# Optimization experiments

Measured on AMD Instinct MI355X. Metric: run time of the kernel, lower is better.

The kernel has to match this reference:

```python
import jax, jax.numpy as jnp
import numpy as np

N_NODES = 100000
N_EDGES = 1600000
IN_DIM = 128
HID = 64
HEADS = 1
NEG_SLOPE = 0.2


def setup_inputs() -> dict:
    key = jax.random.key(0)
    ks = jax.random.split(key, 12)
    def xavier(k, shape):
        fan_in, fan_out = shape[-2], shape[-1]
        lim = jnp.sqrt(6.0 / (fan_in + fan_out))
        return jax.random.uniform(k, shape, jnp.float32, -lim, lim)
    x = jax.random.normal(ks[0], (N_NODES, IN_DIM), jnp.float32)
    edge_index = jax.random.randint(ks[1], (2, N_EDGES), 0, N_NODES, jnp.int64)
    # layer 0: in 128 -> heads*hid (64)
    W0 = xavier(ks[2], (IN_DIM, HEADS * HID))
    al0 = xavier(ks[3], (1, HEADS, HID))
    ar0 = xavier(ks[4], (1, HEADS, HID))
    # layer 1: in heads*hid (64) -> 64
    W1 = xavier(ks[5], (HEADS * HID, HEADS * HID))
    al1 = xavier(ks[6], (1, HEADS, HID))
    ar1 = xavier(ks[7], (1, HEADS, HID))
    # post_mp: Linear(64,64) -> Linear(64,64)
    Wp1 = xavier(ks[8], (HEADS * HID, HID))
    bp1 = jnp.zeros((HID,), jnp.float32)
    Wp2 = xavier(ks[9], (HID, HID))
    bp2 = jnp.zeros((HID,), jnp.float32)
    return {"x": x, "edge_index": edge_index, "W0": W0, "al0": al0, "ar0": ar0,
            "W1": W1, "al1": al1, "ar1": ar1, "Wp1": Wp1, "bp1": bp1,
            "Wp2": Wp2, "bp2": bp2}


def gat_layer(x, W, att_l, att_r, src, dst, n_nodes):
    H, C = att_l.shape[1], att_l.shape[2]
    # lin_l == lin_r (shared weight), no bias
    xh = (x @ W).reshape(n_nodes, H, C)            # [N,H,C]
    alpha_l = jnp.sum(xh * att_l, axis=-1)         # [N,H]
    alpha_r = jnp.sum(xh * att_r, axis=-1)         # [N,H]
    # per-edge logit: alpha_i (dst) + alpha_j (src)
    a = alpha_l[src] + alpha_r[dst]                # [E,H]
    a = jnp.where(a >= 0, a, NEG_SLOPE * a)        # leaky_relu
    # segment softmax over incoming edges of each dst node
    amax = jax.ops.segment_max(a, dst, num_segments=n_nodes)
    e = jnp.exp(a - amax[dst])
    denom = jax.ops.segment_sum(e, dst, num_segments=n_nodes)
    alpha = e / (denom[dst] + 1e-16)               # [E,H]
    msg = xh[src] * alpha[:, :, None]              # [E,H,C]
    out = jax.ops.segment_sum(msg, dst, num_segments=n_nodes)  # [N,H,C]
    return out.reshape(n_nodes, H * C)


def reference(x, edge_index, W0, al0, ar0, W1, al1, ar1, Wp1, bp1, Wp2, bp2):
    src, dst = edge_index[0], edge_index[1]
    n = x.shape[0]
    h = gat_layer(x, W0, al0, ar0, src, dst, n)
    h = jax.nn.relu(h)
    h = gat_layer(h, W1, al1, ar1, src, dst, n)
    h = jax.nn.relu(h)
    # post_mp (dropout inactive in eval)
    h = h @ Wp1 + bp1
    h = h @ Wp2 + bp2
    return h  # emb=True -> return embedding
```

## Files before the change

kernel.cpp:

```cpp
#include <hip/hip_runtime.h>
#include <math.h>

#define NEG_SLOPE 0.2f
#define CAP 8192

typedef _Float16 half8 __attribute__((ext_vector_type(8)));
typedef _Float16 half4v __attribute__((ext_vector_type(4)));
typedef float float4v __attribute__((ext_vector_type(4)));

__global__ void setup_misc(const float* __restrict__ W0, const float* __restrict__ W1,
                           const float* __restrict__ Wp1, const float* __restrict__ Wp2,
                           _Float16* __restrict__ W0T, _Float16* __restrict__ W1T,
                           _Float16* __restrict__ Wp1T, _Float16* __restrict__ Wp2T,
                           int* __restrict__ cursor, int NB) {
    const int tid = threadIdx.x;
    if (blockIdx.x == 4) {
        for (int t = tid; t < NB; t += 256) cursor[t] = t * CAP;
        return;
    }
    __shared__ float lds[128 * 64];
    const float* src; _Float16* dstp; int K;
    switch (blockIdx.x) {
        case 0: src = W0;  dstp = W0T;  K = 128; break;
        case 1: src = W1;  dstp = W1T;  K = 64;  break;
        case 2: src = Wp1; dstp = Wp1T; K = 64;  break;
        default: src = Wp2; dstp = Wp2T; K = 64; break;
    }
    for (int i = tid; i < K * 64; i += 256) lds[i] = src[i];
    __syncthreads();
    for (int i = tid; i < K * 64; i += 256) {
        int n = i / K, k = i % K;
        dstp[i] = (_Float16)lds[k * 64 + n];
    }
}

__device__ __forceinline__ void bin_body(const int* __restrict__ src,
                                         const int* __restrict__ dst,
                                         int* __restrict__ cursor,
                                         unsigned int* __restrict__ packed,
                                         int E, int NB, int bid) {
    __shared__ int h[512];
    const int tid = threadIdx.x;
    for (int t = tid; t < NB; t += 256) h[t] = 0;
    __syncthreads();
    const int base = bid * 4096;
    const int lim = min(base + 4096, E);
    int dreg[16];
    int cnt = 0;
    for (int i = base + tid; i < lim; i += 256) dreg[cnt++] = dst[i];
    for (int k = 0; k < cnt; ++k) atomicAdd(&h[dreg[k] >> 8], 1);
    __syncthreads();
    for (int t = tid; t < NB; t += 256) {
        int c = h[t];
        h[t] = c ? atomicAdd(&cursor[t], c) : 0;
    }
    __syncthreads();
    cnt = 0;
    for (int i = base + tid; i < lim; i += 256) {
        int d = dreg[cnt++];
        int s = src[i];
        int pos = atomicAdd(&h[d >> 8], 1);
        packed[pos] = ((unsigned int)(d & 255) << 24) | (unsigned int)s;
    }
}

__device__ __forceinline__ void gemm0_body(const float* __restrict__ X,
                                           const _Float16* __restrict__ WT,
                                           const float* __restrict__ alw,
                                           const float* __restrict__ arw,
                                           _Float16* __restrict__ XH,
                                           float* __restrict__ AL, float* __restrict__ AR,
                                           int N, int bid) {
    const int wid = threadIdx.x >> 6, lane = threadIdx.x & 63;
    const int rowbase = bid * 64 + wid * 16;
    const int idx16 = lane & 15;
    const int g = lane >> 4;
    const int mrow = rowbase + idx16;
    const bool mvalid = (mrow < N);

    float4v acc[4];
    #pragma unroll
    for (int n = 0; n < 4; ++n) acc[n] = float4v{0.f, 0.f, 0.f, 0.f};

    #pragma unroll
    for (int ks = 0; ks < 4; ++ks) {
        const int k0 = ks * 32 + g * 8;
        half8 a = {};
        if (mvalid) {
            const float* xp = X + (size_t)mrow * 128 + k0;
            float4v lo = *reinterpret_cast<const float4v*>(xp);
            float4v hi = *reinterpret_cast<const float4v*>(xp + 4);
            #pragma unroll
            for (int i = 0; i < 4; ++i) {
                a[i] = (_Float16)lo[i];
                a[i + 4] = (_Float16)hi[i];
            }
        }
        #pragma unroll
        for (int n = 0; n < 4; ++n) {
            const half8 b = *reinterpret_cast<const half8*>(WT + (size_t)(n * 16 + idx16) * 128 + k0);
            acc[n] = __builtin_amdgcn_mfma_f32_16x16x32_f16(a, b, acc[n], 0, 0, 0);
        }
    }

    float alv[4], arv[4];
    #pragma unroll
    for (int n = 0; n < 4; ++n) { alv[n] = alw[n * 16 + idx16]; arv[n] = arw[n * 16 + idx16]; }
    #pragma unroll
    for (int r = 0; r < 4; ++r) {
        const int row = rowbase + g * 4 + r;
        if (row < N) {
            float pl = 0.f, pr = 0.f;
            #pragma unroll
            for (int n = 0; n < 4; ++n) {
                float vv = acc[n][r];
                XH[(size_t)row * 64 + n * 16 + idx16] = (_Float16)vv;
                pl = fmaf(vv, alv[n], pl);
                pr = fmaf(vv, arv[n], pr);
            }
            pl += __shfl_xor(pl, 1); pr += __shfl_xor(pr, 1);
            pl += __shfl_xor(pl, 2); pr += __shfl_xor(pr, 2);
            pl += __shfl_xor(pl, 4); pr += __shfl_xor(pr, 4);
            pl += __shfl_xor(pl, 8); pr += __shfl_xor(pr, 8);
            if (idx16 == 0) { AL[row] = pl; AR[row] = pr; }
        }
    }
}

__global__ void gemm0_and_bin(const float* __restrict__ X,
                              const _Float16* __restrict__ W0T,
                              const float* __restrict__ alw, const float* __restrict__ arw,
                              _Float16* __restrict__ XH0, float* __restrict__ AL0,
                              float* __restrict__ AR0,
                              const int* __restrict__ src, const int* __restrict__ dst,
                              int* __restrict__ cursor, unsigned int* __restrict__ packed,
                              int N, int E, int NB, int geb) {
    if ((int)blockIdx.x < geb)
        bin_body(src, dst, cursor, packed, E, NB, blockIdx.x);
    else
        gemm0_body(X, W0T, alw, arw, XH0, AL0, AR0, N, blockIdx.x - geb);
}

__global__ void bucket_sort(const unsigned int* __restrict__ packed,
                            const int* __restrict__ cursor,
                            int* __restrict__ csr, int2* __restrict__ rr, int N) {
    __shared__ int hist[256], cur[256];
    __shared__ int wsum[4], woff[4];
    const int tid = threadIdx.x, wid = tid >> 6, lane = tid & 63;
    const int b = blockIdx.x;
    const int beg = b * CAP;
    const int end = cursor[b];
    hist[tid] = 0;
    __syncthreads();
    for (int i = beg + tid; i < end; i += 256)
        atomicAdd(&hist[packed[i] >> 24], 1);
    __syncthreads();
    int v = hist[tid];
    int x = v;
    #pragma unroll
    for (int off = 1; off < 64; off <<= 1) {
        int t = __shfl_up(x, off);
        if (lane >= off) x += t;
    }
    if (lane == 63) wsum[wid] = x;
    __syncthreads();
    if (tid == 0) {
        int acc = 0;
        #pragma unroll
        for (int w = 0; w < 4; ++w) { woff[w] = acc; acc += wsum[w]; }
    }
    __syncthreads();
    int excl = woff[wid] + x - v;
    int node = (b << 8) + tid;
    if (node < N) rr[node] = make_int2(beg + excl, v);
    cur[tid] = excl;
    __syncthreads();
    for (int i = beg + tid; i < end; i += 256) {
        unsigned int p = packed[i];
        int pos = atomicAdd(&cur[p >> 24], 1);
        csr[beg + pos] = (int)(p & 0xFFFFFFu);
    }
}


__device__ __forceinline__ void agg_phase(const int2* __restrict__ rr,
                                          const int* __restrict__ csr,
                                          const float* __restrict__ ALp,
                                          const float* __restrict__ ARp,
                                          const _Float16* __restrict__ XHp,
                                          _Float16* ts, int nb, int N) {
    const int tid = threadIdx.x;
    const int l = tid & 15, grp = tid >> 4;
    const int node = nb + grp;
    float4v acc = {0.f, 0.f, 0.f, 0.f};
    float inv = 0.0f;
    if (node < N) {
        const int2 r = rr[node];
        const int beg = r.x, end = r.x + r.y;
        const float ar = ARp[node];
        float s = 0.f;
        for (int cbeg = beg; cbeg < end; cbeg += 16) {
            const int e = cbeg + l;
            const bool valid = (e < end);
            const int sidx = valid ? csr[e] : 0;
            float a = ALp[sidx] + ar;
            a = (a >= 0.0f) ? a : NEG_SLOPE * a;
            const float ex = valid ? __expf(a) : 0.0f;
            s += ex;
            #pragma unroll
            for (int j = 0; j < 16; ++j) {
                const float wgt = __shfl(ex, j, 16);
                const int si = __shfl(sidx, j, 16);
                const half4v h = *reinterpret_cast<const half4v*>(XHp + (size_t)si * 64 + l * 4);
                acc[0] = fmaf((float)h[0], wgt, acc[0]);
                acc[1] = fmaf((float)h[1], wgt, acc[1]);
                acc[2] = fmaf((float)h[2], wgt, acc[2]);
                acc[3] = fmaf((float)h[3], wgt, acc[3]);
            }
        }
        s += __shfl_xor(s, 1); s += __shfl_xor(s, 2);
        s += __shfl_xor(s, 4); s += __shfl_xor(s, 8);
        inv = 1.0f / (s + 1e-16f);
    }
    half4v o;
    o[0] = (_Float16)fmaxf(acc[0] * inv, 0.f);
    o[1] = (_Float16)fmaxf(acc[1] * inv, 0.f);
    o[2] = (_Float16)fmaxf(acc[2] * inv, 0.f);
    o[3] = (_Float16)fmaxf(acc[3] * inv, 0.f);
    const int hoff = (grp * 128 + ((l * 8) ^ ((grp & 7) << 4))) >> 1;
    *reinterpret_cast<half4v*>(ts + hoff) = o;
    __syncthreads();
}

__device__ __forceinline__ half8 ts_afrag(const _Float16* ts, int row, int kb) {
    return *reinterpret_cast<const half8*>(ts + ((row * 128 + (kb ^ ((row & 7) << 4))) >> 1));
}

__global__ void agg_gemm_mid(const int2* __restrict__ rr, const int* __restrict__ csr,
                             const float* __restrict__ AL0, const float* __restrict__ AR0,
                             const _Float16* __restrict__ XH0,
                             const _Float16* __restrict__ W1T,
                             const float* __restrict__ al1w, const float* __restrict__ ar1w,
                             _Float16* __restrict__ XH1, float* __restrict__ AL1,
                             float* __restrict__ AR1, int N) {
    __shared__ _Float16 ts[16 * 64];
    const int nb = blockIdx.x * 16;
    agg_phase(rr, csr, AL0, AR0, XH0, ts, nb, N);
    if (threadIdx.x >= 64) return;

    const int lane = threadIdx.x;
    const int idx16 = lane & 15, g = lane >> 4;
    float alv[4], arv[4];
    #pragma unroll
    for (int n = 0; n < 4; ++n) { alv[n] = al1w[n * 16 + idx16]; arv[n] = ar1w[n * 16 + idx16]; }

    float4v acc[4];
    #pragma unroll
    for (int n = 0; n < 4; ++n) acc[n] = float4v{0.f, 0.f, 0.f, 0.f};
    #pragma unroll
    for (int ks = 0; ks < 2; ++ks) {
        const half8 a = ts_afrag(ts, idx16, ks * 64 + g * 16);
        const int k0 = ks * 32 + g * 8;
        #pragma unroll
        for (int n = 0; n < 4; ++n) {
            const half8 b = *reinterpret_cast<const half8*>(W1T + (size_t)(n * 16 + idx16) * 64 + k0);
            acc[n] = __builtin_amdgcn_mfma_f32_16x16x32_f16(a, b, acc[n], 0, 0, 0);
        }
    }
    #pragma unroll
    for (int r = 0; r < 4; ++r) {
        const int row = nb + g * 4 + r;
        if (row < N) {
            float pl = 0.f, pr = 0.f;
            #pragma unroll
            for (int n = 0; n < 4; ++n) {
                float vv = acc[n][r];
                XH1[(size_t)row * 64 + n * 16 + idx16] = (_Float16)vv;
                pl = fmaf(vv, alv[n], pl);
                pr = fmaf(vv, arv[n], pr);
            }
            pl += __shfl_xor(pl, 1); pr += __shfl_xor(pr, 1);
            pl += __shfl_xor(pl, 2); pr += __shfl_xor(pr, 2);
            pl += __shfl_xor(pl, 4); pr += __shfl_xor(pr, 4);
            pl += __shfl_xor(pl, 8); pr += __shfl_xor(pr, 8);
            if (idx16 == 0) { AL1[row] = pl; AR1[row] = pr; }
        }
    }
}

__global__ void agg_post(const int2* __restrict__ rr, const int* __restrict__ csr,
                         const float* __restrict__ AL1, const float* __restrict__ AR1,
                         const _Float16* __restrict__ XH1,
                         const _Float16* __restrict__ Wp1T, const float* __restrict__ bp1,
                         const _Float16* __restrict__ Wp2T, const float* __restrict__ bp2,
                         float* __restrict__ OUT, int N) {
    __shared__ _Float16 ts[16 * 64];
    __shared__ _Float16 tls[16][72];
    const int nb = blockIdx.x * 16;
    agg_phase(rr, csr, AL1, AR1, XH1, ts, nb, N);
    if (threadIdx.x >= 64) return;

    const int lane = threadIdx.x;
    const int idx16 = lane & 15, g = lane >> 4;

    float4v acc1[4];
    #pragma unroll
    for (int n = 0; n < 4; ++n) acc1[n] = float4v{0.f, 0.f, 0.f, 0.f};
    #pragma unroll
    for (int ks = 0; ks < 2; ++ks) {
        const half8 a = ts_afrag(ts, idx16, ks * 64 + g * 16);
        const int k0 = ks * 32 + g * 8;
        #pragma unroll
        for (int n = 0; n < 4; ++n) {
            const half8 b = *reinterpret_cast<const half8*>(Wp1T + (size_t)(n * 16 + idx16) * 64 + k0);
            acc1[n] = __builtin_amdgcn_mfma_f32_16x16x32_f16(a, b, acc1[n], 0, 0, 0);
        }
    }
    #pragma unroll
    for (int r = 0; r < 4; ++r)
        #pragma unroll
        for (int n = 0; n < 4; ++n)
            tls[g * 4 + r][n * 16 + idx16] = (_Float16)(acc1[n][r] + bp1[n * 16 + idx16]);

    float4v acc2[4];
    #pragma unroll
    for (int n = 0; n < 4; ++n) acc2[n] = float4v{0.f, 0.f, 0.f, 0.f};
    #pragma unroll
    for (int ks = 0; ks < 2; ++ks) {
        const int k0 = ks * 32 + g * 8;
        const half8 a = *reinterpret_cast<const half8*>(&tls[idx16][k0]);
        #pragma unroll
        for (int n = 0; n < 4; ++n) {
            const half8 b = *reinterpret_cast<const half8*>(Wp2T + (size_t)(n * 16 + idx16) * 64 + k0);
            acc2[n] = __builtin_amdgcn_mfma_f32_16x16x32_f16(a, b, acc2[n], 0, 0, 0);
        }
    }
    #pragma unroll
    for (int r = 0; r < 4; ++r) {
        const int row = nb + g * 4 + r;
        if (row < N) {
            #pragma unroll
            for (int n = 0; n < 4; ++n)
                OUT[(size_t)row * 64 + n * 16 + idx16] = acc2[n][r] + bp2[n * 16 + idx16];
        }
    }
}

extern "C" void kernel_launch(void* const* d_in, const int* in_sizes, int n_in,
                              void* d_out, int out_size, void* d_ws, size_t ws_size,
                              hipStream_t stream) {
    const float* x   = (const float*)d_in[0];
    const int*   ei  = (const int*)d_in[1];
    const float* W0  = (const float*)d_in[2];
    const float* al0 = (const float*)d_in[3];
    const float* ar0 = (const float*)d_in[4];
    const float* W1  = (const float*)d_in[5];
    const float* al1 = (const float*)d_in[6];
    const float* ar1 = (const float*)d_in[7];
    const float* Wp1 = (const float*)d_in[8];
    const float* bp1 = (const float*)d_in[9];
    const float* Wp2 = (const float*)d_in[10];
    const float* bp2 = (const float*)d_in[11];
    float* out = (float*)d_out;

    const int N = in_sizes[0] / 128;
    const int E = in_sizes[1] / 2;
    const int* src = ei;
    const int* dst = ei + E;
    const int NB = (N + 255) >> 8;

    char* w = (char*)d_ws;
    _Float16* XH0  = (_Float16*)w;     w += sizeof(_Float16) * (size_t)N * 64;
    _Float16* XH1  = (_Float16*)w;     w += sizeof(_Float16) * (size_t)N * 64;
    float*  AL0    = (float*)w;        w += sizeof(float) * N;
    float*  AR0    = (float*)w;        w += sizeof(float) * N;
    float*  AL1    = (float*)w;        w += sizeof(float) * N;
    float*  AR1    = (float*)w;        w += sizeof(float) * N;
    int2*   rr     = (int2*)w;         w += sizeof(int2) * N;
    int*    csr    = (int*)w;          w += sizeof(int) * (size_t)NB * CAP;
    unsigned int* packed = (unsigned int*)w; w += sizeof(unsigned int) * (size_t)NB * CAP;
    int*    cursor = (int*)w;          w += sizeof(int) * 512;
    _Float16* W0T  = (_Float16*)w;     w += sizeof(_Float16) * 128 * 64;
    _Float16* W1T  = (_Float16*)w;     w += sizeof(_Float16) * 64 * 64;
    _Float16* Wp1T = (_Float16*)w;     w += sizeof(_Float16) * 64 * 64;
    _Float16* Wp2T = (_Float16*)w;

    dim3 blk(256);
    const int gn64 = (N + 63) / 64;
    const int gn16 = (N + 15) / 16;
    const int geb  = (E + 4095) / 4096;

    setup_misc<<<5, blk, 0, stream>>>(W0, W1, Wp1, Wp2, W0T, W1T, Wp1T, Wp2T,
                                      cursor, NB);

    gemm0_and_bin<<<geb + gn64, blk, 0, stream>>>(x, W0T, al0, ar0, XH0, AL0, AR0,
                                                  src, dst, cursor, packed,
                                                  N, E, NB, geb);

    bucket_sort<<<NB, blk, 0, stream>>>(packed, cursor, csr, rr, N);

    agg_gemm_mid<<<gn16, blk, 0, stream>>>(rr, csr, AL0, AR0, XH0,
                                           W1T, al1, ar1, XH1, AL1, AR1, N);

    agg_post<<<gn16, blk, 0, stream>>>(rr, csr, AL1, AR1, XH1,
                                       Wp1T, bp1, Wp2T, bp2, out, N);
}
```

Baseline: 150.5 us.

## Group nodes by degree class via permutation to balance aggregation work

```diff
diff --git a/kernel.cpp b/kernel.cpp
--- a/kernel.cpp
+++ b/kernel.cpp
@@ -12,10 +12,11 @@
                            const float* __restrict__ Wp1, const float* __restrict__ Wp2,
                            _Float16* __restrict__ W0T, _Float16* __restrict__ W1T,
                            _Float16* __restrict__ Wp1T, _Float16* __restrict__ Wp2T,
-                           int* __restrict__ cursor, int NB) {
+                           int* __restrict__ cursor, int* __restrict__ cls16, int NB) {
     const int tid = threadIdx.x;
     if (blockIdx.x == 4) {
         for (int t = tid; t < NB; t += 256) cursor[t] = t * CAP;
+        if (tid < 16) cls16[tid] = 0;
         return;
     }
     __shared__ float lds[128 * 64];
@@ -34,16 +35,14 @@
     }
 }
 
-__device__ __forceinline__ void bin_body(const int* __restrict__ src,
-                                         const int* __restrict__ dst,
-                                         int* __restrict__ cursor,
-                                         unsigned int* __restrict__ packed,
-                                         int E, int NB, int bid) {
+__global__ void bin_k(const int* __restrict__ src, const int* __restrict__ dst,
+                      int* __restrict__ cursor, unsigned int* __restrict__ packed,
+                      int E, int NB) {
     __shared__ int h[512];
     const int tid = threadIdx.x;
     for (int t = tid; t < NB; t += 256) h[t] = 0;
     __syncthreads();
-    const int base = bid * 4096;
+    const int base = blockIdx.x * 4096;
     const int lim = min(base + 4096, E);
     int dreg[16];
     int cnt = 0;
@@ -61,6 +60,51 @@
         int s = src[i];
         int pos = atomicAdd(&h[d >> 8], 1);
         packed[pos] = ((unsigned int)(d & 255) << 24) | (unsigned int)s;
+    }
+}
+
+__device__ __forceinline__ void sort_body(const unsigned int* __restrict__ packed,
+                                          const int* __restrict__ cursor,
+                                          int* __restrict__ csr, int2* __restrict__ rr,
+                                          int* __restrict__ classhist, int N, int b) {
+    __shared__ int hist[256], cur[256];
+    __shared__ int wsum[4], woff[4];
+    __shared__ int chist[8];
+    const int tid = threadIdx.x, wid = tid >> 6, lane = tid & 63;
+    const int beg = b * CAP;
+    const int end = cursor[b];
+    hist[tid] = 0;
+    if (tid < 8) chist[tid] = 0;
+    __syncthreads();
+    for (int i = beg + tid; i < end; i += 256)
+        atomicAdd(&hist[packed[i] >> 24], 1);
+    __syncthreads();
+    int v = hist[tid];
+    const int node = (b << 8) + tid;
+    if (node < N) atomicAdd(&chist[min((v + 15) >> 4, 7)], 1);
+    int x = v;
+    #pragma unroll
+    for (int off = 1; off < 64; off <<= 1) {
+        int t = __shfl_up(x, off);
+        if (lane >= off) x += t;
+    }
+    if (lane == 63) wsum[wid] = x;
+    __syncthreads();
+    if (tid == 0) {
+        int acc = 0;
+        #pragma unroll
+        for (int w = 0; w < 4; ++w) { woff[w] = acc; acc += wsum[w]; }
+    }
+    __syncthreads();
+    if (tid < 8 && chist[tid]) atomicAdd(&classhist[tid], chist[tid]);
+    int excl = woff[wid] + x - v;
+    if (node < N) rr[node] = make_int2(beg + excl, v);
+    cur[tid] = excl;
+    __syncthreads();
+    for (int i = beg + tid; i < end; i += 256) {
+        unsigned int p = packed[i];
+        int pos = atomicAdd(&cur[p >> 24], 1);
+        csr[beg + pos] = (int)(p & 0xFFFFFFu);
     }
 }
 
@@ -127,74 +171,64 @@
     }
 }
 
-__global__ void gemm0_and_bin(const float* __restrict__ X,
-                              const _Float16* __restrict__ W0T,
-                              const float* __restrict__ alw, const float* __restrict__ arw,
-                              _Float16* __restrict__ XH0, float* __restrict__ AL0,
-                              float* __restrict__ AR0,
-                              const int* __restrict__ src, const int* __restrict__ dst,
-                              int* __restrict__ cursor, unsigned int* __restrict__ packed,
-                              int N, int E, int NB, int geb) {
-    if ((int)blockIdx.x < geb)
-        bin_body(src, dst, cursor, packed, E, NB, blockIdx.x);
+__global__ void sort_and_gemm0(const unsigned int* __restrict__ packed,
+                               const int* __restrict__ cursor,
+                               int* __restrict__ csr, int2* __restrict__ rr,
+                               int* __restrict__ classhist,
+                               const float* __restrict__ X,
+                               const _Float16* __restrict__ W0T,
+                               const float* __restrict__ alw, const float* __restrict__ arw,
+                               _Float16* __restrict__ XH0, float* __restrict__ AL0,
+                               float* __restrict__ AR0, int N, int NB) {
+    if ((int)blockIdx.x < NB)
+        sort_body(packed, cursor, csr, rr, classhist, N, blockIdx.x);
     else
-        gemm0_body(X, W0T, alw, arw, XH0, AL0, AR0, N, blockIdx.x - geb);
-}
-
-__global__ void bucket_sort(const unsigned int* __restrict__ packed,
-                            const int* __restrict__ cursor,
-                            int* __restrict__ csr, int2* __restrict__ rr, int N) {
-    __shared__ int hist[256], cur[256];
-    __shared__ int wsum[4], woff[4];
-    const int tid = threadIdx.x, wid = tid >> 6, lane = tid & 63;
-    const int b = blockIdx.x;
-    const int beg = b * CAP;
-    const int end = cursor[b];
-    hist[tid] = 0;
-    __syncthreads();
-    for (int i = beg + tid; i < end; i += 256)
-        atomicAdd(&hist[packed[i] >> 24], 1);
-    __syncthreads();
-    int v = hist[tid];
-    int x = v;
-    #pragma unroll
-    for (int off = 1; off < 64; off <<= 1) {
-        int t = __shfl_up(x, off);
-        if (lane >= off) x += t;
-    }
-    if (lane == 63) wsum[wid] = x;
-    __syncthreads();
-    if (tid == 0) {
-        int acc = 0;
-        #pragma unroll
-        for (int w = 0; w < 4; ++w) { woff[w] = acc; acc += wsum[w]; }
-    }
-    __syncthreads();
-    int excl = woff[wid] + x - v;
-    int node = (b << 8) + tid;
-    if (node < N) rr[node] = make_int2(beg + excl, v);
-    cur[tid] = excl;
-    __syncthreads();
-    for (int i = beg + tid; i < end; i += 256) {
-        unsigned int p = packed[i];
-        int pos = atomicAdd(&cur[p >> 24], 1);
-        csr[beg + pos] = (int)(p & 0xFFFFFFu);
+        gemm0_body(X, W0T, alw, arw, XH0, AL0, AR0, N, blockIdx.x - NB);
+}
+
+__global__ void class_scatter(const int2* __restrict__ rr,
+                              const int* __restrict__ classhist,
+                              int* __restrict__ classOffset,
+                              int* __restrict__ perm, int N) {
+    __shared__ int h[8], cur[8];
+    const int tid = threadIdx.x;
+    const int node = blockIdx.x * 256 + tid;
+    if (tid < 8) h[tid] = 0;
+    __syncthreads();
+    int c = -1;
+    if (node < N) {
+        c = min((rr[node].y + 15) >> 4, 7);
+        atomicAdd(&h[c], 1);
+    }
+    __syncthreads();
+    if (tid < 8) {
+        int cnt = h[tid];
+        cur[tid] = cnt ? atomicAdd(&classOffset[tid], cnt) : 0;
+    }
+    __syncthreads();
+    if (node < N) {
+        int cb = 0;
+        for (int k = 0; k < c; ++k) cb += classhist[k];
+        int pos = cb + atomicAdd(&cur[c], 1);
+        perm[pos] = node;
     }
 }
 
 
 __device__ __forceinline__ void agg_phase(const int2* __restrict__ rr,
                                           const int* __restrict__ csr,
+                                          const int* __restrict__ perm,
                                           const float* __restrict__ ALp,
                                           const float* __restrict__ ARp,
                                           const _Float16* __restrict__ XHp,
                                           _Float16* ts, int nb, int N) {
     const int tid = threadIdx.x;
     const int l = tid & 15, grp = tid >> 4;
-    const int node = nb + grp;
+    const int nidx = nb + grp;
     float4v acc = {0.f, 0.f, 0.f, 0.f};
     float inv = 0.0f;
-    if (node < N) {
+    if (nidx < N) {
+        const int node = perm[nidx];
         const int2 r = rr[node];
         const int beg = r.x, end = r.x + r.y;
         const float ar = ARp[node];
@@ -237,6 +271,7 @@
 }
 
 __global__ void agg_gemm_mid(const int2* __restrict__ rr, const int* __restrict__ csr,
+                             const int* __restrict__ perm,
                              const float* __restrict__ AL0, const float* __restrict__ AR0,
                              const _Float16* __restrict__ XH0,
                              const _Float16* __restrict__ W1T,
@@ -245,7 +280,7 @@
                              float* __restrict__ AR1, int N) {
     __shared__ _Float16 ts[16 * 64];
     const int nb = blockIdx.x * 16;
-    agg_phase(rr, csr, AL0, AR0, XH0, ts, nb, N);
+    agg_phase(rr, csr, perm, AL0, AR0, XH0, ts, nb, N);
     if (threadIdx.x >= 64) return;
 
     const int lane = threadIdx.x;
@@ -269,13 +304,14 @@
     }
     #pragma unroll
     for (int r = 0; r < 4; ++r) {
-        const int row = nb + g * 4 + r;
-        if (row < N) {
+        const int idx = nb + g * 4 + r;
+        if (idx < N) {
+            const int prow = perm[idx];
             float pl = 0.f, pr = 0.f;
             #pragma unroll
             for (int n = 0; n < 4; ++n) {
                 float vv = acc[n][r];
-                XH1[(size_t)row * 64 + n * 16 + idx16] = (_Float16)vv;
+                XH1[(size_t)prow * 64 + n * 16 + idx16] = (_Float16)vv;
                 pl = fmaf(vv, alv[n], pl);
                 pr = fmaf(vv, arv[n], pr);
             }
@@ -283,12 +319,13 @@
             pl += __shfl_xor(pl, 2); pr += __shfl_xor(pr, 2);
             pl += __shfl_xor(pl, 4); pr += __shfl_xor(pr, 4);
             pl += __shfl_xor(pl, 8); pr += __shfl_xor(pr, 8);
-            if (idx16 == 0) { AL1[row] = pl; AR1[row] = pr; }
+            if (idx16 == 0) { AL1[prow] = pl; AR1[prow] = pr; }
         }
     }
 }
 
 __global__ void agg_post(const int2* __restrict__ rr, const int* __restrict__ csr,
+                         const int* __restrict__ perm,
                          const float* __restrict__ AL1, const float* __restrict__ AR1,
                          const _Float16* __restrict__ XH1,
                          const _Float16* __restrict__ Wp1T, const float* __restrict__ bp1,
@@ -297,7 +334,7 @@
     __shared__ _Float16 ts[16 * 64];
     __shared__ _Float16 tls[16][72];
     const int nb = blockIdx.x * 16;
-    agg_phase(rr, csr, AL1, AR1, XH1, ts, nb, N);
+    agg_phase(rr, csr, perm, AL1, AR1, XH1, ts, nb, N);
     if (threadIdx.x >= 64) return;
 
     const int lane = threadIdx.x;
@@ -337,11 +374,12 @@
     }
     #pragma unroll
     for (int r = 0; r < 4; ++r) {
-        const int row = nb + g * 4 + r;
-        if (row < N) {
+        const int idx = nb + g * 4 + r;
+        if (idx < N) {
+            const int prow = perm[idx];
             #pragma unroll
             for (int n = 0; n < 4; ++n)
-                OUT[(size_t)row * 64 + n * 16 + idx16] = acc2[n][r] + bp2[n * 16 + idx16];
+                OUT[(size_t)prow * 64 + n * 16 + idx16] = acc2[n][r] + bp2[n * 16 + idx16];
         }
     }
 }
@@ -380,28 +418,35 @@
     int*    csr    = (int*)w;          w += sizeof(int) * (size_t)NB * CAP;
     unsigned int* packed = (unsigned int*)w; w += sizeof(unsigned int) * (size_t)NB * CAP;
     int*    cursor = (int*)w;          w += sizeof(int) * 512;
+    int*    cls16  = (int*)w;          w += sizeof(int) * 16;
+    int*    perm   = (int*)w;          w += sizeof(int) * N;
     _Float16* W0T  = (_Float16*)w;     w += sizeof(_Float16) * 128 * 64;
     _Float16* W1T  = (_Float16*)w;     w += sizeof(_Float16) * 64 * 64;
     _Float16* Wp1T = (_Float16*)w;     w += sizeof(_Float16) * 64 * 64;
     _Float16* Wp2T = (_Float16*)w;
+    int* classhist   = cls16;
+    int* classOffset = cls16 + 8;
 
     dim3 blk(256);
     const int gn64 = (N + 63) / 64;
     const int gn16 = (N + 15) / 16;
+    const int gn256 = (N + 255) / 256;
     const int geb  = (E + 4095) / 4096;
 
     setup_misc<<<5, blk, 0, stream>>>(W0, W1, Wp1, Wp2, W0T, W1T, Wp1T, Wp2T,
-                                      cursor, NB);
-
-    gemm0_and_bin<<<geb + gn64, blk, 0, stream>>>(x, W0T, al0, ar0, XH0, AL0, AR0,
-                                                  src, dst, cursor, packed,
-                                                  N, E, NB, geb);
-
-    bucket_sort<<<NB, blk, 0, stream>>>(packed, cursor, csr, rr, N);
-
-    agg_gemm_mid<<<gn16, blk, 0, stream>>>(rr, csr, AL0, AR0, XH0,
+                                      cursor, cls16, NB);
+
+    bin_k<<<geb, blk, 0, stream>>>(src, dst, cursor, packed, E, NB);
+
+    sort_and_gemm0<<<NB + gn64, blk, 0, stream>>>(packed, cursor, csr, rr, classhist,
+                                                  x, W0T, al0, ar0, XH0, AL0, AR0,
+                                                  N, NB);
+
+    class_scatter<<<gn256, blk, 0, stream>>>(rr, classhist, classOffset, perm, N);
+
+    agg_gemm_mid<<<gn16, blk, 0, stream>>>(rr, csr, perm, AL0, AR0, XH0,
                                            W1T, al1, ar1, XH1, AL1, AR1, N);
 
-    agg_post<<<gn16, blk, 0, stream>>>(rr, csr, AL1, AR1, XH1,
+    agg_post<<<gn16, blk, 0, stream>>>(rr, csr, perm, AL1, AR1, XH1,
                                        Wp1T, bp1, Wp2T, bp2, out, N);
 }
```

Measured after the change: 155.8 us. 1.04x slower.

## Reorder nodes by in-degree class within buckets to balance aggregation groups

Applied to the files above, without the earlier changes.

```diff
diff --git a/kernel.cpp b/kernel.cpp
--- a/kernel.cpp
+++ b/kernel.cpp
@@ -143,19 +143,29 @@
 
 __global__ void bucket_sort(const unsigned int* __restrict__ packed,
                             const int* __restrict__ cursor,
-                            int* __restrict__ csr, int2* __restrict__ rr, int N) {
+                            int* __restrict__ csr, int2* __restrict__ rr,
+                            int* __restrict__ perm, int N) {
     __shared__ int hist[256], cur[256];
     __shared__ int wsum[4], woff[4];
+    __shared__ int chist[8], coff[8], crank[8];
     const int tid = threadIdx.x, wid = tid >> 6, lane = tid & 63;
     const int b = blockIdx.x;
     const int beg = b * CAP;
     const int end = cursor[b];
     hist[tid] = 0;
+    if (tid < 8) { chist[tid] = 0; crank[tid] = 0; }
     __syncthreads();
     for (int i = beg + tid; i < end; i += 256)
         atomicAdd(&hist[packed[i] >> 24], 1);
     __syncthreads();
-    int v = hist[tid];
+    const int v = hist[tid];
+    const int node = (b << 8) + tid;
+    const int c = min((v + 15) >> 4, 7);
+    int rank = 0;
+    if (node < N) {
+        atomicAdd(&chist[c], 1);
+        rank = atomicAdd(&crank[c], 1);
+    }
     int x = v;
     #pragma unroll
     for (int off = 1; off < 64; off <<= 1) {
@@ -168,11 +178,16 @@
         int acc = 0;
         #pragma unroll
         for (int w = 0; w < 4; ++w) { woff[w] = acc; acc += wsum[w]; }
+        acc = 0;
+        #pragma unroll
+        for (int k = 0; k < 8; ++k) { coff[k] = acc; acc += chist[k]; }
     }
     __syncthreads();
     int excl = woff[wid] + x - v;
-    int node = (b << 8) + tid;
-    if (node < N) rr[node] = make_int2(beg + excl, v);
+    if (node < N) {
+        rr[node] = make_int2(beg + excl, v);
+        perm[(b << 8) + coff[c] + rank] = node;
+    }
     cur[tid] = excl;
     __syncthreads();
     for (int i = beg + tid; i < end; i += 256) {
@@ -185,16 +200,18 @@
 
 __device__ __forceinline__ void agg_phase(const int2* __restrict__ rr,
                                           const int* __restrict__ csr,
+                                          const int* __restrict__ perm,
                                           const float* __restrict__ ALp,
                                           const float* __restrict__ ARp,
                                           const _Float16* __restrict__ XHp,
                                           _Float16* ts, int nb, int N) {
     const int tid = threadIdx.x;
     const int l = tid & 15, grp = tid >> 4;
-    const int node = nb + grp;
+    const int nidx = nb + grp;
     float4v acc = {0.f, 0.f, 0.f, 0.f};
     float inv = 0.0f;
-    if (node < N) {
+    if (nidx < N) {
+        const int node = perm[nidx];
         const int2 r = rr[node];
         const int beg = r.x, end = r.x + r.y;
         const float ar = ARp[node];
@@ -237,6 +254,7 @@
 }
 
 __global__ void agg_gemm_mid(const int2* __restrict__ rr, const int* __restrict__ csr,
+                             const int* __restrict__ perm,
                              const float* __restrict__ AL0, const float* __restrict__ AR0,
                              const _Float16* __restrict__ XH0,
                              const _Float16* __restrict__ W1T,
@@ -245,7 +263,7 @@
                              float* __restrict__ AR1, int N) {
     __shared__ _Float16 ts[16 * 64];
     const int nb = blockIdx.x * 16;
-    agg_phase(rr, csr, AL0, AR0, XH0, ts, nb, N);
+    agg_phase(rr, csr, perm, AL0, AR0, XH0, ts, nb, N);
     if (threadIdx.x >= 64) return;
 
     const int lane = threadIdx.x;
@@ -269,13 +287,14 @@
     }
     #pragma unroll
     for (int r = 0; r < 4; ++r) {
-        const int row = nb + g * 4 + r;
-        if (row < N) {
+        const int idx = nb + g * 4 + r;
+        if (idx < N) {
+            const int prow = perm[idx];
             float pl = 0.f, pr = 0.f;
             #pragma unroll
             for (int n = 0; n < 4; ++n) {
                 float vv = acc[n][r];
-                XH1[(size_t)row * 64 + n * 16 + idx16] = (_Float16)vv;
+                XH1[(size_t)prow * 64 + n * 16 + idx16] = (_Float16)vv;
                 pl = fmaf(vv, alv[n], pl);
                 pr = fmaf(vv, arv[n], pr);
             }
@@ -283,12 +302,13 @@
             pl += __shfl_xor(pl, 2); pr += __shfl_xor(pr, 2);
             pl += __shfl_xor(pl, 4); pr += __shfl_xor(pr, 4);
             pl += __shfl_xor(pl, 8); pr += __shfl_xor(pr, 8);
-            if (idx16 == 0) { AL1[row] = pl; AR1[row] = pr; }
+            if (idx16 == 0) { AL1[prow] = pl; AR1[prow] = pr; }
         }
     }
 }
 
 __global__ void agg_post(const int2* __restrict__ rr, const int* __restrict__ csr,
+                         const int* __restrict__ perm,
                          const float* __restrict__ AL1, const float* __restrict__ AR1,
                          const _Float16* __restrict__ XH1,
                          const _Float16* __restrict__ Wp1T, const float* __restrict__ bp1,
@@ -297,7 +317,7 @@
     __shared__ _Float16 ts[16 * 64];
     __shared__ _Float16 tls[16][72];
     const int nb = blockIdx.x * 16;
-    agg_phase(rr, csr, AL1, AR1, XH1, ts, nb, N);
+    agg_phase(rr, csr, perm, AL1, AR1, XH1, ts, nb, N);
     if (threadIdx.x >= 64) return;
 
     const int lane = threadIdx.x;
@@ -337,11 +357,12 @@
     }
     #pragma unroll
     for (int r = 0; r < 4; ++r) {
-        const int row = nb + g * 4 + r;
-        if (row < N) {
+        const int idx = nb + g * 4 + r;
+        if (idx < N) {
+            const int prow = perm[idx];
             #pragma unroll
             for (int n = 0; n < 4; ++n)
-                OUT[(size_t)row * 64 + n * 16 + idx16] = acc2[n][r] + bp2[n * 16 + idx16];
+                OUT[(size_t)prow * 64 + n * 16 + idx16] = acc2[n][r] + bp2[n * 16 + idx16];
         }
     }
 }
@@ -380,6 +401,7 @@
     int*    csr    = (int*)w;          w += sizeof(int) * (size_t)NB * CAP;
     unsigned int* packed = (unsigned int*)w; w += sizeof(unsigned int) * (size_t)NB * CAP;
     int*    cursor = (int*)w;          w += sizeof(int) * 512;
+    int*    perm   = (int*)w;          w += sizeof(int) * (size_t)NB * 256;
     _Float16* W0T  = (_Float16*)w;     w += sizeof(_Float16) * 128 * 64;
     _Float16* W1T  = (_Float16*)w;     w += sizeof(_Float16) * 64 * 64;
     _Float16* Wp1T = (_Float16*)w;     w += sizeof(_Float16) * 64 * 64;
@@ -397,11 +419,11 @@
                                                   src, dst, cursor, packed,
                                                   N, E, NB, geb);
 
-    bucket_sort<<<NB, blk, 0, stream>>>(packed, cursor, csr, rr, N);
-
-    agg_gemm_mid<<<gn16, blk, 0, stream>>>(rr, csr, AL0, AR0, XH0,
+    bucket_sort<<<NB, blk, 0, stream>>>(packed, cursor, csr, rr, perm, N);
+
+    agg_gemm_mid<<<gn16, blk, 0, stream>>>(rr, csr, perm, AL0, AR0, XH0,
                                            W1T, al1, ar1, XH1, AL1, AR1, N);
 
-    agg_post<<<gn16, blk, 0, stream>>>(rr, csr, AL1, AR1, XH1,
+    agg_post<<<gn16, blk, 0, stream>>>(rr, csr, perm, AL1, AR1, XH1,
                                        Wp1T, bp1, Wp2T, bp2, out, N);
 }
```

New measurement: 157.8 us. 4.9% more time.

## Stage edge binning through LDS for coalesced writes and fuse sort with gemm0

Applied to the files above, without the earlier changes.

```diff
diff --git a/kernel.cpp b/kernel.cpp
--- a/kernel.cpp
+++ b/kernel.cpp
@@ -34,33 +34,88 @@
     }
 }
 
-__device__ __forceinline__ void bin_body(const int* __restrict__ src,
-                                         const int* __restrict__ dst,
-                                         int* __restrict__ cursor,
-                                         unsigned int* __restrict__ packed,
-                                         int E, int NB, int bid) {
-    __shared__ int h[512];
+__global__ void bin_staged(const int* __restrict__ src, const int* __restrict__ dst,
+                           int* __restrict__ cursor, unsigned int* __restrict__ packed,
+                           int E, int NB) {
+    __shared__ unsigned int sval[4096];
+    __shared__ unsigned int saddr[4096];
+    __shared__ int h[512], hcur[512], gb[512];
+    __shared__ int stot;
     const int tid = threadIdx.x;
+    if (tid == 0) stot = 0;
     for (int t = tid; t < NB; t += 256) h[t] = 0;
     __syncthreads();
-    const int base = bid * 4096;
+    const int base = blockIdx.x * 4096;
     const int lim = min(base + 4096, E);
-    int dreg[16];
+    int dreg[16], sreg[16];
     int cnt = 0;
-    for (int i = base + tid; i < lim; i += 256) dreg[cnt++] = dst[i];
+    for (int i = base + tid; i < lim; i += 256) {
+        dreg[cnt] = dst[i];
+        sreg[cnt] = src[i];
+        ++cnt;
+    }
     for (int k = 0; k < cnt; ++k) atomicAdd(&h[dreg[k] >> 8], 1);
     __syncthreads();
     for (int t = tid; t < NB; t += 256) {
         int c = h[t];
-        h[t] = c ? atomicAdd(&cursor[t], c) : 0;
-    }
-    __syncthreads();
-    cnt = 0;
-    for (int i = base + tid; i < lim; i += 256) {
-        int d = dreg[cnt++];
-        int s = src[i];
-        int pos = atomicAdd(&h[d >> 8], 1);
-        packed[pos] = ((unsigned int)(d & 255) << 24) | (unsigned int)s;
+        if (c) {
+            int l = atomicAdd(&stot, c);
+            hcur[t] = l;
+            gb[t] = atomicAdd(&cursor[t], c) - l;
+        }
+    }
+    __syncthreads();
+    for (int k = 0; k < cnt; ++k) {
+        const int d = dreg[k];
+        const int b = d >> 8;
+        const int pos = atomicAdd(&hcur[b], 1);
+        sval[pos] = ((unsigned int)(d & 255) << 24) | (unsigned int)sreg[k];
+        saddr[pos] = (unsigned int)(gb[b] + pos);
+    }
+    __syncthreads();
+    const int tot = stot;
+    for (int j = tid; j < tot; j += 256)
+        packed[saddr[j]] = sval[j];
+}
+
+__device__ __forceinline__ void sort_body(const unsigned int* __restrict__ packed,
+                                          const int* __restrict__ cursor,
+                                          int* __restrict__ csr, int2* __restrict__ rr,
+                                          int N, int b) {
+    __shared__ int hist[256], cur[256];
+    __shared__ int wsum[4], woff[4];
+    const int tid = threadIdx.x, wid = tid >> 6, lane = tid & 63;
+    const int beg = b * CAP;
+    const int end = cursor[b];
+    hist[tid] = 0;
+    __syncthreads();
+    for (int i = beg + tid; i < end; i += 256)
+        atomicAdd(&hist[packed[i] >> 24], 1);
+    __syncthreads();
+    int v = hist[tid];
+    int x = v;
+    #pragma unroll
+    for (int off = 1; off < 64; off <<= 1) {
+        int t = __shfl_up(x, off);
+        if (lane >= off) x += t;
+    }
+    if (lane == 63) wsum[wid] = x;
+    __syncthreads();
+    if (tid == 0) {
+        int acc = 0;
+        #pragma unroll
+        for (int w = 0; w < 4; ++w) { woff[w] = acc; acc += wsum[w]; }
+    }
+    __syncthreads();
+    int excl = woff[wid] + x - v;
+    int node = (b << 8) + tid;
+    if (node < N) rr[node] = make_int2(beg + excl, v);
+    cur[tid] = excl;
+    __syncthreads();
+    for (int i = beg + tid; i < end; i += 256) {
+        unsigned int p = packed[i];
+        int pos = atomicAdd(&cur[p >> 24], 1);
+        csr[beg + pos] = (int)(p & 0xFFFFFFu);
     }
 }
 
@@ -127,59 +182,18 @@
     }
 }
 
-__global__ void gemm0_and_bin(const float* __restrict__ X,
-                              const _Float16* __restrict__ W0T,
-                              const float* __restrict__ alw, const float* __restrict__ arw,
-                              _Float16* __restrict__ XH0, float* __restrict__ AL0,
-                              float* __restrict__ AR0,
-                              const int* __restrict__ src, const int* __restrict__ dst,
-                              int* __restrict__ cursor, unsigned int* __restrict__ packed,
-                              int N, int E, int NB, int geb) {
-    if ((int)blockIdx.x < geb)
-        bin_body(src, dst, cursor, packed, E, NB, blockIdx.x);
+__global__ void sort_and_gemm0(const unsigned int* __restrict__ packed,
+                               const int* __restrict__ cursor,
+                               int* __restrict__ csr, int2* __restrict__ rr,
+                               const float* __restrict__ X,
+                               const _Float16* __restrict__ W0T,
+                               const float* __restrict__ alw, const float* __restrict__ arw,
+                               _Float16* __restrict__ XH0, float* __restrict__ AL0,
+                               float* __restrict__ AR0, int N, int NB) {
+    if ((int)blockIdx.x < NB)
+        sort_body(packed, cursor, csr, rr, N, blockIdx.x);
     else
-        gemm0_body(X, W0T, alw, arw, XH0, AL0, AR0, N, blockIdx.x - geb);
-}
-
-__global__ void bucket_sort(const unsigned int* __restrict__ packed,
-                            const int* __restrict__ cursor,
-                            int* __restrict__ csr, int2* __restrict__ rr, int N) {
-    __shared__ int hist[256], cur[256];
-    __shared__ int wsum[4], woff[4];
-    const int tid = threadIdx.x, wid = tid >> 6, lane = tid & 63;
-    const int b = blockIdx.x;
-    const int beg = b * CAP;
-    const int end = cursor[b];
-    hist[tid] = 0;
-    __syncthreads();
-    for (int i = beg + tid; i < end; i += 256)
-        atomicAdd(&hist[packed[i] >> 24], 1);
-    __syncthreads();
-    int v = hist[tid];
-    int x = v;
-    #pragma unroll
-    for (int off = 1; off < 64; off <<= 1) {
-        int t = __shfl_up(x, off);
-        if (lane >= off) x += t;
-    }
-    if (lane == 63) wsum[wid] = x;
-    __syncthreads();
-    if (tid == 0) {
-        int acc = 0;
-        #pragma unroll
-        for (int w = 0; w < 4; ++w) { woff[w] = acc; acc += wsum[w]; }
-    }
-    __syncthreads();
-    int excl = woff[wid] + x - v;
-    int node = (b << 8) + tid;
-    if (node < N) rr[node] = make_int2(beg + excl, v);
-    cur[tid] = excl;
-    __syncthreads();
-    for (int i = beg + tid; i < end; i += 256) {
-        unsigned int p = packed[i];
-        int pos = atomicAdd(&cur[p >> 24], 1);
-        csr[beg + pos] = (int)(p & 0xFFFFFFu);
-    }
+        gemm0_body(X, W0T, alw, arw, XH0, AL0, AR0, N, blockIdx.x - NB);
 }
 
 
@@ -393,11 +407,11 @@
     setup_misc<<<5, blk, 0, stream>>>(W0, W1, Wp1, Wp2, W0T, W1T, Wp1T, Wp2T,
                                       cursor, NB);
 
-    gemm0_and_bin<<<geb + gn64, blk, 0, stream>>>(x, W0T, al0, ar0, XH0, AL0, AR0,
-                                                  src, dst, cursor, packed,
-                                                  N, E, NB, geb);
-
-    bucket_sort<<<NB, blk, 0, stream>>>(packed, cursor, csr, rr, N);
+    bin_staged<<<geb, blk, 0, stream>>>(src, dst, cursor, packed, E, NB);
+
+    sort_and_gemm0<<<NB + gn64, blk, 0, stream>>>(packed, cursor, csr, rr,
+                                                  x, W0T, al0, ar0, XH0, AL0, AR0,
+                                                  N, NB);
 
     agg_gemm_mid<<<gn16, blk, 0, stream>>>(rr, csr, AL0, AR0, XH0,
                                            W1T, al1, ar1, XH1, AL1, AR1, N);
```

After: 151.9 us. About the same (+1.0%).
